# Performance work log

Measured on AMD Instinct MI355X. Metric: run time of the kernel, lower is better.

The kernel has to match this reference:

```python
import jax, jax.numpy as jnp
import numpy as np

EMBED = 1024
HIDDEN = 64  # embed_size // n_heads
B, L = 8, 4096


def setup_inputs() -> dict:
    key = jax.random.key(0)
    k1, k2, k3, k4, k5, k6, k7 = jax.random.split(key, 7)
    query = jax.random.normal(k1, (B, L, EMBED), dtype=jnp.float32)
    key_t = jax.random.normal(k2, (B, L, EMBED), dtype=jnp.float32)
    value = jax.random.normal(k3, (B, L, EMBED), dtype=jnp.float32)
    mask = jax.random.randint(k4, (B, L, L), 0, 2).astype(jnp.bool_)
    # nn.Linear(embed, hidden, bias=False) weights have shape (hidden, embed)
    s = 1.0 / np.sqrt(EMBED)
    WQ = jax.random.uniform(k5, (HIDDEN, EMBED), jnp.float32, -s, s)
    WK = jax.random.uniform(k6, (HIDDEN, EMBED), jnp.float32, -s, s)
    WV = jax.random.uniform(k7, (HIDDEN, EMBED), jnp.float32, -s, s)
    return {"query": query, "key": key_t, "value": value, "mask": mask,
            "WQ": WQ, "WK": WK, "WV": WV}


def reference(query, key, value, mask, WQ, WK, WV):
    # Projections: y = x @ W.T  (Linear without bias)
    Q = jnp.einsum('ble,he->blh', query, WQ)   # [B,L,H]
    K = jnp.einsum('ble,he->blh', key, WK)
    V = jnp.einsum('ble,he->blh', value, WV)
    scale = 1.0 / jnp.sqrt(jnp.asarray(Q.shape[-1], Q.dtype))
    scores = jnp.einsum('bqh,bkh->bqk', Q, K) * scale   # [B,L,L]
    scores = jnp.where(mask, -jnp.inf, scores)
    attn = jax.nn.softmax(scores, axis=-1)
    # dropout p=0.0 -> identity
    return jnp.einsum('bqk,bkh->bqh', attn, V)           # [B,L,H]
```

## Files before the change

### kernel.cpp

```cpp
#include <hip/hip_runtime.h>
#include <hip/hip_bf16.h>

#define NB 8
#define LL 4096
#define EE 1024
#define HH 64

typedef unsigned short u16;
typedef unsigned char u8;
typedef unsigned int u32;
typedef unsigned long long u64;
using bf16x8 = __attribute__((ext_vector_type(8))) short;
using bf16x4 = __attribute__((ext_vector_type(4))) short;
using f32x4  = __attribute__((ext_vector_type(4))) float;

__device__ __forceinline__ short f2bf(float f) {
    __hip_bfloat16 h = __float2bfloat16(f);
    return __builtin_bit_cast(short, h);
}

__device__ __forceinline__ bf16x8 pack8(const float4 a, const float4 b) {
    bf16x8 r;
    r[0] = f2bf(a.x); r[1] = f2bf(a.y); r[2] = f2bf(a.z); r[3] = f2bf(a.w);
    r[4] = f2bf(b.x); r[5] = f2bf(b.y); r[6] = f2bf(b.z); r[7] = f2bf(b.w);
    return r;
}

__global__ __launch_bounds__(256) void proj_kernel(
    const float* __restrict__ Xq, const float* __restrict__ Xk, const float* __restrict__ Xv,
    const float* __restrict__ Wq, const float* __restrict__ Wk, const float* __restrict__ Wv,
    u16* __restrict__ Oq, u16* __restrict__ Ok, u16* __restrict__ Ovt)
{
    __shared__ u16 Xs[2][64][72];
    __shared__ u16 Ws2[2][64][72];

    const int which = blockIdx.y;
    const float* X = (which == 0) ? Xq : (which == 1) ? Xk : Xv;
    const float* W = (which == 0) ? Wq : (which == 1) ? Wk : Wv;
    const float scale = (which == 0) ? 0.125f : 1.0f;

    const int tid  = threadIdx.x;
    const int lane = tid & 63;
    const int w    = tid >> 6;
    const int g    = lane >> 4;
    const int c    = lane & 15;
    const int m0   = blockIdx.x * 64;
    const int r    = tid >> 2;
    const int cb   = (tid & 3) * 16;

    const float* xrow = X + (size_t)(m0 + r) * EE + cb;
    const float* wrow = W + (size_t)r * EE + cb;

    float4 xr[4], wr[4];
    #pragma unroll
    for (int i = 0; i < 4; ++i) {
        xr[i] = reinterpret_cast<const float4*>(xrow)[i];
        wr[i] = reinterpret_cast<const float4*>(wrow)[i];
    }
    *reinterpret_cast<bf16x8*>(&Xs[0][r][cb])      = pack8(xr[0], xr[1]);
    *reinterpret_cast<bf16x8*>(&Xs[0][r][cb + 8])  = pack8(xr[2], xr[3]);
    *reinterpret_cast<bf16x8*>(&Ws2[0][r][cb])     = pack8(wr[0], wr[1]);
    *reinterpret_cast<bf16x8*>(&Ws2[0][r][cb + 8]) = pack8(wr[2], wr[3]);
    __syncthreads();

    f32x4 acc[4];
    #pragma unroll
    for (int t = 0; t < 4; ++t) acc[t] = (f32x4){0.f, 0.f, 0.f, 0.f};

    for (int s = 0; s < 16; ++s) {
        const int curb = s & 1, nxtb = curb ^ 1;
        if (s < 15) {
            #pragma unroll
            for (int i = 0; i < 4; ++i) {
                xr[i] = reinterpret_cast<const float4*>(xrow + (s + 1) * 64)[i];
                wr[i] = reinterpret_cast<const float4*>(wrow + (s + 1) * 64)[i];
            }
        }
        __builtin_amdgcn_s_setprio(1);
        #pragma unroll
        for (int kk = 0; kk < 2; ++kk) {
            bf16x8 a = *reinterpret_cast<const bf16x8*>(&Xs[curb][16*w + c][kk*32 + 8*g]);
            #pragma unroll
            for (int t = 0; t < 4; ++t) {
                bf16x8 bb = *reinterpret_cast<const bf16x8*>(&Ws2[curb][16*t + c][kk*32 + 8*g]);
                acc[t] = __builtin_amdgcn_mfma_f32_16x16x32_bf16(a, bb, acc[t], 0, 0, 0);
            }
        }
        __builtin_amdgcn_s_setprio(0);
        if (s < 15) {
            *reinterpret_cast<bf16x8*>(&Xs[nxtb][r][cb])      = pack8(xr[0], xr[1]);
            *reinterpret_cast<bf16x8*>(&Xs[nxtb][r][cb + 8])  = pack8(xr[2], xr[3]);
            *reinterpret_cast<bf16x8*>(&Ws2[nxtb][r][cb])     = pack8(wr[0], wr[1]);
            *reinterpret_cast<bf16x8*>(&Ws2[nxtb][r][cb + 8]) = pack8(wr[2], wr[3]);
        }
        __syncthreads();
    }

    if (which < 2) {
        u16* O = (which == 0) ? Oq : Ok;
        #pragma unroll
        for (int t = 0; t < 4; ++t)
            #pragma unroll
            for (int q = 0; q < 4; ++q) {
                const int mrow = m0 + 16*w + 4*g + q;
                O[(size_t)mrow * HH + 16*t + c] = (u16)f2bf(acc[t][q] * scale);
            }
    } else {
        const int bidx = m0 >> 12;
        #pragma unroll
        for (int t = 0; t < 4; ++t)
            #pragma unroll
            for (int q = 0; q < 4; ++q) {
                const int l = (m0 & (LL - 1)) + 16*w + 4*g + q;
                Ovt[((size_t)bidx * HH + 16*t + c) * LL + l] = (u16)f2bf(acc[t][q]);
            }
    }
}

__global__ __launch_bounds__(256) void attn_kernel(
    const u16* __restrict__ Qb, const u16* __restrict__ Kb, const u16* __restrict__ Vt,
    const int* __restrict__ mask, float* __restrict__ out)
{
    __shared__ u16 Ks[2][64][72];
    __shared__ u16 Vts[2][64][72];
    __shared__ u16 Pt[4][16][72];
    __shared__ u64 Pnl[2][4][64];

    const int b    = blockIdx.y;
    const int q0   = blockIdx.x * 64;
    const int tid  = threadIdx.x;
    const int lane = tid & 63;
    const int w    = tid >> 6;
    const int g    = lane >> 4;
    const int c    = lane & 15;
    const int r    = tid >> 2;
    const int cb   = (tid & 3) * 16;
    const int mrr  = tid >> 4;
    const int mcc  = tid & 15;

    const u16* kbase = Kb + (size_t)b * LL * HH;
    const u16* vbase = Vt + (size_t)b * HH * LL;
    const int* mbase0 = mask + (size_t)b * LL * LL + (size_t)(q0 + mrr) * LL + mcc * 16;

    bf16x8 qf[2];
    {
        const u16* qp = Qb + ((size_t)b * LL + q0 + 16*w + c) * HH;
        qf[0] = *reinterpret_cast<const bf16x8*>(qp + 8*g);
        qf[1] = *reinterpret_cast<const bf16x8*>(qp + 32 + 8*g);
    }

    bf16x8 kra, krb, vra, vrb;
    int4 mi0, mi1, mi2, mi3;

    #define LOADKV(kt_) do {                                                   \
        kra = *reinterpret_cast<const bf16x8*>(kbase + (size_t)((kt_)*64 + r) * HH + cb);       \
        krb = *reinterpret_cast<const bf16x8*>(kbase + (size_t)((kt_)*64 + r) * HH + cb + 8);   \
        vra = *reinterpret_cast<const bf16x8*>(vbase + (size_t)r * LL + (kt_)*64 + cb);         \
        vrb = *reinterpret_cast<const bf16x8*>(vbase + (size_t)r * LL + (kt_)*64 + cb + 8);     \
    } while (0)
    #define WRITEKV(buf_) do {                                                 \
        *reinterpret_cast<bf16x8*>(&Ks[buf_][r][cb])      = kra;               \
        *reinterpret_cast<bf16x8*>(&Ks[buf_][r][cb + 8])  = krb;               \
        *reinterpret_cast<bf16x8*>(&Vts[buf_][r][cb])     = vra;               \
        *reinterpret_cast<bf16x8*>(&Vts[buf_][r][cb + 8]) = vrb;               \
    } while (0)
    #define MLOAD(w_, p_) do {                                                 \
        const int4* _mp = reinterpret_cast<const int4*>(mbase0 + (size_t)(16*(p_)) * LL + (w_)*256); \
        mi0 = _mp[0]; mi1 = _mp[1]; mi2 = _mp[2]; mi3 = _mp[3];                \
    } while (0)
    #define MPACK(pb_, p_) do {                                                \
        u32 _bb =  (u32)(mi0.x != 0)        | ((u32)(mi0.y != 0) << 1)         \
                | ((u32)(mi0.z != 0) << 2)  | ((u32)(mi0.w != 0) << 3)         \
                | ((u32)(mi1.x != 0) << 4)  | ((u32)(mi1.y != 0) << 5)         \
                | ((u32)(mi1.z != 0) << 6)  | ((u32)(mi1.w != 0) << 7)         \
                | ((u32)(mi2.x != 0) << 8)  | ((u32)(mi2.y != 0) << 9)         \
                | ((u32)(mi2.z != 0) << 10) | ((u32)(mi2.w != 0) << 11)        \
                | ((u32)(mi3.x != 0) << 12) | ((u32)(mi3.y != 0) << 13)        \
                | ((u32)(mi3.z != 0) << 14) | ((u32)(mi3.w != 0) << 15);       \
        ((u16*)&Pnl[pb_][mcc >> 2][16*(p_) + mrr])[mcc & 3] = (u16)_bb;        \
    } while (0)

    f32x4 accT[4];
    float lpart = 0.f;
    #pragma unroll
    for (int t = 0; t < 4; ++t) accT[t] = (f32x4){0.f, 0.f, 0.f, 0.f};

    #define TILE_BODY(CUR, PB, TI) do {                                        \
        f32x4 s[4];                                                            \
        __builtin_amdgcn_s_setprio(1);                                         \
        _Pragma("unroll")                                                      \
        for (int tp = 0; tp < 4; ++tp) {                                       \
            s[tp] = (f32x4){0.f, 0.f, 0.f, 0.f};                               \
            _Pragma("unroll")                                                  \
            for (int kk = 0; kk < 2; ++kk) {                                   \
                bf16x8 afr = *reinterpret_cast<const bf16x8*>(&Ks[CUR][16*tp + c][kk*32 + 8*g]);\
                s[tp] = __builtin_amdgcn_mfma_f32_16x16x32_bf16(afr, qf[kk], s[tp], 0, 0, 0);   \
            }                                                                  \
        }                                                                      \
        __builtin_amdgcn_s_setprio(0);                                         \
        u64 mw = Pnl[PB][TI][16*w + c];                                        \
        u32 mlo = (u32)mw, mhi = (u32)(mw >> 32);                              \
        _Pragma("unroll")                                                      \
        for (int tp = 0; tp < 4; ++tp) {                                       \
            u32 wsel = (tp < 2) ? mlo : mhi;                                   \
            bf16x4 pk;                                                         \
            _Pragma("unroll")                                                  \
            for (int qq = 0; qq < 4; ++qq) {                                   \
                u32 bit = (wsel >> ((tp & 1) * 16 + 4*g + qq)) & 1u;           \
                float p = bit ? 0.f : __expf(s[tp][qq]);                       \
                lpart += p;                                                    \
                pk[qq] = f2bf(p);                                              \
            }                                                                  \
            *reinterpret_cast<bf16x4*>(&Pt[w][c][16*tp + 4*g]) = pk;           \
        }                                                                      \
        __builtin_amdgcn_s_setprio(1);                                         \
        _Pragma("unroll")                                                      \
        for (int kk = 0; kk < 2; ++kk) {                                       \
            bf16x8 pfr = *reinterpret_cast<const bf16x8*>(&Pt[w][c][kk*32 + 8*g]);              \
            _Pragma("unroll")                                                  \
            for (int u = 0; u < 4; ++u) {                                      \
                bf16x8 vfr = *reinterpret_cast<const bf16x8*>(&Vts[CUR][16*u + c][kk*32 + 8*g]);\
                accT[u] = __builtin_amdgcn_mfma_f32_16x16x32_bf16(vfr, pfr, accT[u], 0, 0, 0);  \
            }                                                                  \
        }                                                                      \
        __builtin_amdgcn_s_setprio(0);                                         \
    } while (0)

    LOADKV(0);
    MLOAD(0, 0); MPACK(0, 0);
    MLOAD(0, 1); MPACK(0, 1);
    MLOAD(0, 2); MPACK(0, 2);
    MLOAD(0, 3); MPACK(0, 3);
    WRITEKV(0);
    __syncthreads();

    for (int win = 0; win < 16; ++win) {
        const int base = 4 * win;
        const int pcur = win & 1, pnxt = pcur ^ 1;
        const bool more = (win + 1 < 16);

        LOADKV(base + 1);
        if (more) MLOAD(win + 1, 0);
        TILE_BODY(0, pcur, 0);
        WRITEKV(1);
        if (more) MPACK(pnxt, 0);
        __syncthreads();

        LOADKV(base + 2);
        if (more) MLOAD(win + 1, 1);
        TILE_BODY(1, pcur, 1);
        WRITEKV(0);
        if (more) MPACK(pnxt, 1);
        __syncthreads();

        LOADKV(base + 3);
        if (more) MLOAD(win + 1, 2);
        TILE_BODY(0, pcur, 2);
        WRITEKV(1);
        if (more) MPACK(pnxt, 2);
        __syncthreads();

        if (more) { LOADKV(base + 4); MLOAD(win + 1, 3); }
        TILE_BODY(1, pcur, 3);
        if (more) { WRITEKV(0); MPACK(pnxt, 3); }
        __syncthreads();
    }

    lpart += __shfl_xor(lpart, 16, 64);
    lpart += __shfl_xor(lpart, 32, 64);
    const float inv = 1.0f / lpart;
    const size_t row = (size_t)b * LL + q0 + 16*w + c;
    #pragma unroll
    for (int u = 0; u < 4; ++u) {
        float4 v;
        v.x = accT[u][0] * inv;
        v.y = accT[u][1] * inv;
        v.z = accT[u][2] * inv;
        v.w = accT[u][3] * inv;
        *reinterpret_cast<float4*>(&out[row * HH + 16*u + 4*g]) = v;
    }
}

extern "C" void kernel_launch(void* const* d_in, const int* in_sizes, int n_in,
                              void* d_out, int out_size, void* d_ws, size_t ws_size,
                              hipStream_t stream) {
    const float* query = (const float*)d_in[0];
    const float* key_t = (const float*)d_in[1];
    const float* value = (const float*)d_in[2];
    const int*   mask  = (const int*)d_in[3];
    const float* WQ    = (const float*)d_in[4];
    const float* WK    = (const float*)d_in[5];
    const float* WV    = (const float*)d_in[6];
    float* out = (float*)d_out;

    const size_t nqkv = (size_t)NB * LL * HH;
    u16* Qb  = (u16*)d_ws;
    u16* Kb  = Qb + nqkv;
    u16* Vtb = Kb + nqkv;

    dim3 pgrid(NB * LL / 64, 3);
    proj_kernel<<<pgrid, 256, 0, stream>>>(query, key_t, value, WQ, WK, WV, Qb, Kb, Vtb);

    dim3 agrid(LL / 64, NB);
    attn_kernel<<<agrid, 256, 0, stream>>>(Qb, Kb, Vtb, mask, out);
}
```

Before: 216.6 us.

## Deepen global prefetch to two tiles ahead with register double buffers

The K/V tile loads now run two tiles ahead using even/odd register sets, and the mask loads run one step further ahead, so global latency has more compute to hide behind. The __syncthreads calls are replaced by a custom barrier that waits only on LDS counters (lgkmcnt) and fences the scheduler, so outstanding global loads need not drain at each barrier. This costs more registers, which may lower occupancy, and depends on the hand-written waitcnt being correct.

```diff
diff --git a/kernel.cpp b/kernel.cpp
--- a/kernel.cpp
+++ b/kernel.cpp
@@ -149,35 +149,56 @@
         qf[1] = *reinterpret_cast<const bf16x8*>(qp + 32 + 8*g);
     }
 
-    bf16x8 kra, krb, vra, vrb;
-    int4 mi0, mi1, mi2, mi3;
-
-    #define LOADKV(kt_) do {                                                   \
-        kra = *reinterpret_cast<const bf16x8*>(kbase + (size_t)((kt_)*64 + r) * HH + cb);       \
-        krb = *reinterpret_cast<const bf16x8*>(kbase + (size_t)((kt_)*64 + r) * HH + cb + 8);   \
-        vra = *reinterpret_cast<const bf16x8*>(vbase + (size_t)r * LL + (kt_)*64 + cb);         \
-        vrb = *reinterpret_cast<const bf16x8*>(vbase + (size_t)r * LL + (kt_)*64 + cb + 8);     \
-    } while (0)
-    #define WRITEKV(buf_) do {                                                 \
-        *reinterpret_cast<bf16x8*>(&Ks[buf_][r][cb])      = kra;               \
-        *reinterpret_cast<bf16x8*>(&Ks[buf_][r][cb + 8])  = krb;               \
-        *reinterpret_cast<bf16x8*>(&Vts[buf_][r][cb])     = vra;               \
-        *reinterpret_cast<bf16x8*>(&Vts[buf_][r][cb + 8]) = vrb;               \
-    } while (0)
-    #define MLOAD(w_, p_) do {                                                 \
-        const int4* _mp = reinterpret_cast<const int4*>(mbase0 + (size_t)(16*(p_)) * LL + (w_)*256); \
-        mi0 = _mp[0]; mi1 = _mp[1]; mi2 = _mp[2]; mi3 = _mp[3];                \
-    } while (0)
-    #define MPACK(pb_, p_) do {                                                \
-        u32 _bb =  (u32)(mi0.x != 0)        | ((u32)(mi0.y != 0) << 1)         \
-                | ((u32)(mi0.z != 0) << 2)  | ((u32)(mi0.w != 0) << 3)         \
-                | ((u32)(mi1.x != 0) << 4)  | ((u32)(mi1.y != 0) << 5)         \
-                | ((u32)(mi1.z != 0) << 6)  | ((u32)(mi1.w != 0) << 7)         \
-                | ((u32)(mi2.x != 0) << 8)  | ((u32)(mi2.y != 0) << 9)         \
-                | ((u32)(mi2.z != 0) << 10) | ((u32)(mi2.w != 0) << 11)        \
-                | ((u32)(mi3.x != 0) << 12) | ((u32)(mi3.y != 0) << 13)        \
-                | ((u32)(mi3.z != 0) << 14) | ((u32)(mi3.w != 0) << 15);       \
-        ((u16*)&Pnl[pb_][mcc >> 2][16*(p_) + mrr])[mcc & 3] = (u16)_bb;        \
+    #define BARRIER() do {                                                     \
+        asm volatile("s_waitcnt lgkmcnt(0)" ::: "memory");                     \
+        __builtin_amdgcn_sched_barrier(0);                                     \
+        __builtin_amdgcn_s_barrier();                                          \
+        __builtin_amdgcn_sched_barrier(0);                                     \
+    } while (0)
+
+    bf16x8 kEa, kEb, vEa, vEb;
+    bf16x8 kOa, kOb, vOa, vOb;
+    int4 mA0, mA1, mA2, mA3, mB0, mB1, mB2, mB3;
+
+    #define LOADKV_E(kt_) do {                                                 \
+        kEa = *reinterpret_cast<const bf16x8*>(kbase + (size_t)((kt_)*64 + r) * HH + cb);       \
+        kEb = *reinterpret_cast<const bf16x8*>(kbase + (size_t)((kt_)*64 + r) * HH + cb + 8);   \
+        vEa = *reinterpret_cast<const bf16x8*>(vbase + (size_t)r * LL + (kt_)*64 + cb);         \
+        vEb = *reinterpret_cast<const bf16x8*>(vbase + (size_t)r * LL + (kt_)*64 + cb + 8);     \
+    } while (0)
+    #define LOADKV_O(kt_) do {                                                 \
+        kOa = *reinterpret_cast<const bf16x8*>(kbase + (size_t)((kt_)*64 + r) * HH + cb);       \
+        kOb = *reinterpret_cast<const bf16x8*>(kbase + (size_t)((kt_)*64 + r) * HH + cb + 8);   \
+        vOa = *reinterpret_cast<const bf16x8*>(vbase + (size_t)r * LL + (kt_)*64 + cb);         \
+        vOb = *reinterpret_cast<const bf16x8*>(vbase + (size_t)r * LL + (kt_)*64 + cb + 8);     \
+    } while (0)
+    #define WRITEKV_E(buf_) do {                                               \
+        *reinterpret_cast<bf16x8*>(&Ks[buf_][r][cb])      = kEa;               \
+        *reinterpret_cast<bf16x8*>(&Ks[buf_][r][cb + 8])  = kEb;               \
+        *reinterpret_cast<bf16x8*>(&Vts[buf_][r][cb])     = vEa;               \
+        *reinterpret_cast<bf16x8*>(&Vts[buf_][r][cb + 8]) = vEb;               \
+    } while (0)
+    #define WRITEKV_O(buf_) do {                                               \
+        *reinterpret_cast<bf16x8*>(&Ks[buf_][r][cb])      = kOa;               \
+        *reinterpret_cast<bf16x8*>(&Ks[buf_][r][cb + 8])  = kOb;               \
+        *reinterpret_cast<bf16x8*>(&Vts[buf_][r][cb])     = vOa;               \
+        *reinterpret_cast<bf16x8*>(&Vts[buf_][r][cb + 8]) = vOb;               \
+    } while (0)
+    #define MLOADX(P0, P1, P2, P3, sg) do {                                    \
+        const int4* _mp = reinterpret_cast<const int4*>(                       \
+            mbase0 + (size_t)(16 * ((sg) & 3)) * LL + ((sg) >> 2) * 256);      \
+        P0 = _mp[0]; P1 = _mp[1]; P2 = _mp[2]; P3 = _mp[3];                    \
+    } while (0)
+    #define MPACKX(P0, P1, P2, P3, sg) do {                                    \
+        u32 _bb =  (u32)(P0.x != 0)        | ((u32)(P0.y != 0) << 1)           \
+                | ((u32)(P0.z != 0) << 2)  | ((u32)(P0.w != 0) << 3)           \
+                | ((u32)(P1.x != 0) << 4)  | ((u32)(P1.y != 0) << 5)           \
+                | ((u32)(P1.z != 0) << 6)  | ((u32)(P1.w != 0) << 7)           \
+                | ((u32)(P2.x != 0) << 8)  | ((u32)(P2.y != 0) << 9)           \
+                | ((u32)(P2.z != 0) << 10) | ((u32)(P2.w != 0) << 11)          \
+                | ((u32)(P3.x != 0) << 12) | ((u32)(P3.y != 0) << 13)          \
+                | ((u32)(P3.z != 0) << 14) | ((u32)(P3.w != 0) << 15);         \
+        ((u16*)&Pnl[((sg) >> 2) & 1][mcc >> 2][16 * ((sg) & 3) + mrr])[mcc & 3] = (u16)_bb; \
     } while (0)
 
     f32x4 accT[4];
@@ -226,44 +247,33 @@
         __builtin_amdgcn_s_setprio(0);                                         \
     } while (0)
 
-    LOADKV(0);
-    MLOAD(0, 0); MPACK(0, 0);
-    MLOAD(0, 1); MPACK(0, 1);
-    MLOAD(0, 2); MPACK(0, 2);
-    MLOAD(0, 3); MPACK(0, 3);
-    WRITEKV(0);
-    __syncthreads();
-
-    for (int win = 0; win < 16; ++win) {
-        const int base = 4 * win;
-        const int pcur = win & 1, pnxt = pcur ^ 1;
-        const bool more = (win + 1 < 16);
-
-        LOADKV(base + 1);
-        if (more) MLOAD(win + 1, 0);
-        TILE_BODY(0, pcur, 0);
-        WRITEKV(1);
-        if (more) MPACK(pnxt, 0);
-        __syncthreads();
-
-        LOADKV(base + 2);
-        if (more) MLOAD(win + 1, 1);
-        TILE_BODY(1, pcur, 1);
-        WRITEKV(0);
-        if (more) MPACK(pnxt, 1);
-        __syncthreads();
-
-        LOADKV(base + 3);
-        if (more) MLOAD(win + 1, 2);
-        TILE_BODY(0, pcur, 2);
-        WRITEKV(1);
-        if (more) MPACK(pnxt, 2);
-        __syncthreads();
-
-        if (more) { LOADKV(base + 4); MLOAD(win + 1, 3); }
-        TILE_BODY(1, pcur, 3);
-        if (more) { WRITEKV(0); MPACK(pnxt, 3); }
-        __syncthreads();
+    LOADKV_E(0);
+    MLOADX(mA0, mA1, mA2, mA3, 0); MPACKX(mA0, mA1, mA2, mA3, 0);
+    MLOADX(mA0, mA1, mA2, mA3, 1); MPACKX(mA0, mA1, mA2, mA3, 1);
+    MLOADX(mA0, mA1, mA2, mA3, 2); MPACKX(mA0, mA1, mA2, mA3, 2);
+    MLOADX(mA0, mA1, mA2, mA3, 3); MPACKX(mA0, mA1, mA2, mA3, 3);
+    WRITEKV_E(0);
+    LOADKV_O(1);
+    MLOADX(mB0, mB1, mB2, mB3, 4);
+    BARRIER();
+
+    for (int it = 0; it < 32; ++it) {
+        const int f0 = 2 * it;
+        const int f1 = f0 + 1;
+
+        if (f0 + 2 < 64) LOADKV_E(f0 + 2);
+        if (f0 + 5 < 64) MLOADX(mA0, mA1, mA2, mA3, f0 + 5);
+        TILE_BODY(0, (f0 >> 2) & 1, f0 & 3);
+        WRITEKV_O(1);
+        if (f0 + 4 < 64) MPACKX(mB0, mB1, mB2, mB3, f0 + 4);
+        BARRIER();
+
+        if (f1 + 2 < 64) LOADKV_O(f1 + 2);
+        if (f1 + 5 < 64) MLOADX(mB0, mB1, mB2, mB3, f1 + 5);
+        TILE_BODY(1, (f1 >> 2) & 1, f1 & 3);
+        if (f1 + 1 < 64) WRITEKV_E(0);
+        if (f1 + 4 < 64) MPACKX(mA0, mA1, mA2, mA3, f1 + 4);
+        BARRIER();
     }
 
     lpart += __shfl_xor(lpart, 16, 64);
```

Result: no change. 219.7 us (+1.5%).
